# Kernel optimization log

Hardware: AMD Instinct MI355X
Metric: run time of the kernel (lower is better)

The kernel has to match this reference:

```python
import jax, jax.numpy as jnp
import numpy as np

N = 100000   # nodes
E = 1600000  # directed edges
F_IN = 100
H = 256
N_LABELS = 19
BN_EPS = 1e-5


def setup_inputs() -> dict:
    key = jax.random.key(0)
    ks = jax.random.split(key, 12)
    p = lambda k, shape, s=0.05: jax.random.normal(k, shape, dtype=jnp.float32) * s
    return {
        "x": jax.random.normal(ks[0], (N, F_IN), dtype=jnp.float32),
        "edge_index": jax.random.randint(ks[1], (2, E), 0, N, dtype=jnp.int32),
        "W1": p(ks[2], (F_IN, F_IN)), "b1": jnp.zeros((F_IN,), jnp.float32),
        "W2": p(ks[3], (F_IN, F_IN)), "b2": jnp.zeros((F_IN,), jnp.float32),
        "W3": p(ks[4], (F_IN, H)),   "b3": jnp.zeros((H,), jnp.float32),
        "fc1_W": p(ks[5], (H, H)),   "fc1_b": jnp.zeros((H,), jnp.float32),
        "fc2a_W": p(ks[6], (H, 128)), "fc2a_b": jnp.zeros((128,), jnp.float32),
        "bn_gamma": jnp.ones((128,), jnp.float32), "bn_beta": jnp.zeros((128,), jnp.float32),
        "fc2b_W": p(ks[7], (128, N_LABELS)), "fc2b_b": jnp.zeros((N_LABELS,), jnp.float32),
    }


def _gcn_conv(x, W, b, src, dst, dinv):
    """PyG GCNConv with add_self_loops + symmetric normalization.
    out[dst] += dinv[src]*dinv[dst] * (x @ W)[src], plus self-loop term, plus bias.
    """
    n = x.shape[0]
    xw = x @ W  # [N, out]
    norm = dinv[src] * dinv[dst]  # [E]
    agg = jax.ops.segment_sum(xw[src] * norm[:, None], dst, num_segments=n)
    agg = agg + xw * (dinv * dinv)[:, None]  # self loops (i -> i)
    return agg + b


def reference(x, edge_index, W1, b1, W2, b2, W3, b3, fc1_W, fc1_b,
              fc2a_W, fc2a_b, bn_gamma, bn_beta, fc2b_W, fc2b_b):
    src, dst = edge_index[0], edge_index[1]
    n = x.shape[0]
    # degree of augmented graph (A + I), computed on targets (sum aggregation)
    deg = jax.ops.segment_sum(jnp.ones((src.shape[0],), x.dtype), dst, num_segments=n) + 1.0
    dinv = jax.lax.rsqrt(deg)

    h = jnp.clip(x, -0.4, 0.4)
    h = jax.nn.relu(_gcn_conv(h, W1, b1, src, dst, dinv))
    h = jax.nn.relu(_gcn_conv(h, W2, b2, src, dst, dinv))
    h = jax.nn.relu(_gcn_conv(h, W3, b3, src, dst, dinv))
    h = jax.nn.relu(h @ fc1_W + fc1_b)
    # fc2: Linear -> BatchNorm1d (train mode, batch stats) -> ReLU -> Linear
    h = h @ fc2a_W + fc2a_b
    mu = jnp.mean(h, axis=0)
    var = jnp.mean(jnp.square(h - mu), axis=0)  # biased var, as torch BN uses
    h = (h - mu) * jax.lax.rsqrt(var + BN_EPS) * bn_gamma + bn_beta
    h = jax.nn.relu(h)
    logits = h @ fc2b_W + fc2b_b
    return jax.nn.log_softmax(logits, axis=1)
```

## Files before the change

kernel.cpp:

```cpp
#include <hip/hip_runtime.h>
#include <hip/hip_bf16.h>

#define N_NODES 100000
#define N_EDGES 1600000
#define F_IN_DIM 100
#define F_IN_PAD 104
#define H_DIM 256
#define BN_DIM 128
#define N_LABELS 19
#define BN_EPS 1e-5f
#define M_PAD 100096

#define BUCKET_SHIFT 8
#define NB 391
#define EPB 4096
#define PB 391

typedef __attribute__((ext_vector_type(8))) short bf16x8;
typedef __attribute__((ext_vector_type(4))) short s16x4;
typedef __attribute__((ext_vector_type(4))) float f32x4;

static __device__ inline short f2bf(float f) {
    __hip_bfloat16 h = __float2bfloat16(f);
    return *(short*)&h;
}
static __device__ inline float bf2f(short s) {
    unsigned u = ((unsigned)(unsigned short)s) << 16;
    return __builtin_bit_cast(float, u);
}

#define GLOAD_LDS16(g, l) \
    __builtin_amdgcn_global_load_lds((__attribute__((address_space(1))) const unsigned int*)(g), \
                                     (__attribute__((address_space(3))) unsigned int*)(l), 16, 0, 0)

__global__ __launch_bounds__(256) void part_hist_kernel(const int* __restrict__ dst,
                                                        int* __restrict__ part_hist, int E)
{
    __shared__ int h[NB];
    int tid = threadIdx.x;
    for (int i = tid; i < NB; i += 256) h[i] = 0;
    __syncthreads();
    int base = blockIdx.x * EPB;
    int end = min(base + EPB, E);
    for (int e = base + tid; e < end; e += 256)
        atomicAdd(&h[dst[e] >> BUCKET_SHIFT], 1);
    __syncthreads();
    for (int i = tid; i < NB; i += 256) part_hist[blockIdx.x * NB + i] = h[i];
}

__global__ __launch_bounds__(512) void bucket_total_kernel(const int* __restrict__ part_hist,
                                                           int* __restrict__ bucket_total)
{
    __shared__ int ls[512];
    int b = blockIdx.x;
    int s = 0;
    for (int p = threadIdx.x; p < PB; p += 512) s += part_hist[p * NB + b];
    ls[threadIdx.x] = s;
    __syncthreads();
    for (int off = 256; off > 0; off >>= 1) {
        if (threadIdx.x < off) ls[threadIdx.x] += ls[threadIdx.x + off];
        __syncthreads();
    }
    if (threadIdx.x == 0) bucket_total[b] = ls[0];
}

__global__ __launch_bounds__(512) void bucket_scan_kernel(const int* __restrict__ bucket_total,
                                                          int* __restrict__ bucket_base)
{
    __shared__ int ls[512];
    int tid = threadIdx.x;
    ls[tid] = (tid < NB) ? bucket_total[tid] : 0;
    __syncthreads();
    for (int off = 1; off < 512; off <<= 1) {
        int v = ls[tid];
        int add = (tid >= off) ? ls[tid - off] : 0;
        __syncthreads();
        ls[tid] = v + add;
        __syncthreads();
    }
    if (tid < NB) bucket_base[tid] = (tid > 0) ? ls[tid - 1] : 0;
    if (tid == 0) bucket_base[NB] = ls[NB - 1];
}

__global__ __launch_bounds__(512) void part_offset_kernel(int* __restrict__ part_hist,
                                                          const int* __restrict__ bucket_base)
{
    __shared__ int ls[512];
    int b = blockIdx.x;
    int tid = threadIdx.x;
    int v = (tid < PB) ? part_hist[tid * NB + b] : 0;
    ls[tid] = v;
    __syncthreads();
    for (int off = 1; off < 512; off <<= 1) {
        int x = ls[tid];
        int add = (tid >= off) ? ls[tid - off] : 0;
        __syncthreads();
        ls[tid] = x + add;
        __syncthreads();
    }
    if (tid < PB) part_hist[tid * NB + b] = bucket_base[b] + ((tid > 0) ? ls[tid - 1] : 0);
}

__global__ __launch_bounds__(256) void partition_kernel(const int* __restrict__ src,
                                                        const int* __restrict__ dst,
                                                        const int* __restrict__ part_hist,
                                                        int* __restrict__ ep, int E)
{
    __shared__ int cur[NB];
    int tid = threadIdx.x;
    for (int i = tid; i < NB; i += 256) cur[i] = part_hist[blockIdx.x * NB + i];
    __syncthreads();
    int base = blockIdx.x * EPB;
    int end = min(base + EPB, E);
    for (int e = base + tid; e < end; e += 256) {
        int d = dst[e];
        int s = src[e];
        int pos = atomicAdd(&cur[d >> BUCKET_SHIFT], 1);
        ep[pos] = (s << 8) | (d & 255);
    }
}

__global__ __launch_bounds__(256) void bucket_csr_kernel(const int* __restrict__ ep,
                                                         const int* __restrict__ bucket_base,
                                                         int* __restrict__ row_start,
                                                         float* __restrict__ dinv,
                                                         int* __restrict__ src_sorted, int N, int E)
{
    __shared__ int h[256], sc[256], cur[256];
    int b = blockIdx.x;
    int tid = threadIdx.x;
    int e0 = bucket_base[b], e1 = bucket_base[b + 1];
    int node0 = b << BUCKET_SHIFT;
    int nn = min(256, N - node0);

    h[tid] = 0;
    __syncthreads();
    for (int e = e0 + tid; e < e1; e += 256)
        atomicAdd(&h[ep[e] & 255], 1);
    __syncthreads();

    sc[tid] = h[tid];
    __syncthreads();
    for (int off = 1; off < 256; off <<= 1) {
        int v = sc[tid];
        int add = (tid >= off) ? sc[tid - off] : 0;
        __syncthreads();
        sc[tid] = v + add;
        __syncthreads();
    }
    int excl = e0 + ((tid > 0) ? sc[tid - 1] : 0);
    if (tid < nn) {
        row_start[node0 + tid] = excl;
        dinv[node0 + tid] = rsqrtf((float)h[tid] + 1.0f);
    }
    cur[tid] = excl;
    __syncthreads();
    for (int e = e0 + tid; e < e1; e += 256) {
        int p = ep[e];
        int pos = atomicAdd(&cur[p & 255], 1);
        src_sorted[pos] = ((unsigned)p) >> 8;
    }
    if (b == 0 && tid == 0) row_start[N] = E;
}

__global__ __launch_bounds__(256) void pack_all(
    const float* __restrict__ W1, const float* __restrict__ W2, const float* __restrict__ W3,
    const float* __restrict__ Wf1, const float* __restrict__ Wf2a,
    short* __restrict__ Wt1, short* __restrict__ Wt2, short* __restrict__ Wt3,
    short* __restrict__ Wtf1, short* __restrict__ Wtf2a)
{
    int idx = blockIdx.x * 256 + threadIdx.x;
    const float* W; short* Wt; int K, N, Kp, local;
    if (idx < 10400)       { W = W1;   Wt = Wt1;   K = 100; N = 100; Kp = 104; local = idx; }
    else if (idx < 20800)  { W = W2;   Wt = Wt2;   K = 100; N = 100; Kp = 104; local = idx - 10400; }
    else if (idx < 47424)  { W = W3;   Wt = Wt3;   K = 100; N = 256; Kp = 104; local = idx - 20800; }
    else if (idx < 112960) { W = Wf1;  Wt = Wtf1;  K = 256; N = 256; Kp = 256; local = idx - 47424; }
    else if (idx < 145728) { W = Wf2a; Wt = Wtf2a; K = 256; N = 128; Kp = 256; local = idx - 112960; }
    else return;
    int n = local / Kp, k = local - n * Kp;
    Wt[local] = (k < K) ? f2bf(W[(size_t)k * N + n]) : (short)0;
}

template<int ABF16>
__global__ __launch_bounds__(256) void gemm_oneshot(
    const void* __restrict__ Av, const short* __restrict__ Wt,
    const float* __restrict__ bias, const float* __restrict__ rowscale,
    short* __restrict__ C, int M, int Nout, int strideA, int strideC, int relu)
{
    __shared__ __align__(16) short As[128][F_IN_PAD];
    __shared__ __align__(16) short Bs[128][F_IN_PAD];
    int tid = threadIdx.x;
    int rowBase = blockIdx.x * 128;
    int colBase = blockIdx.y * 128;

    if (ABF16) {
        const short* A = (const short*)Av;
        for (int ch = tid; ch < 128 * 13; ch += 256) {
            int r = ch / 13, c8 = (ch - r * 13) * 8;
            int gr = rowBase + r;
            bf16x8 o = (bf16x8){0,0,0,0,0,0,0,0};
            if (gr < M) o = *(const bf16x8*)(A + (size_t)gr * strideA + c8);
            *(bf16x8*)(&As[r][c8]) = o;
        }
    } else {
        const float* A = (const float*)Av;
        for (int ch = tid; ch < 128 * 25; ch += 256) {
            int r = ch / 25, c4 = (ch - r * 25) * 4;
            int gr = rowBase + r;
            float4 v = make_float4(0.f, 0.f, 0.f, 0.f);
            if (gr < M) v = *(const float4*)(A + (size_t)gr * strideA + c4);
            v.x = fminf(fmaxf(v.x, -0.4f), 0.4f);
            v.y = fminf(fmaxf(v.y, -0.4f), 0.4f);
            v.z = fminf(fmaxf(v.z, -0.4f), 0.4f);
            v.w = fminf(fmaxf(v.w, -0.4f), 0.4f);
            s16x4 o = (s16x4){f2bf(v.x), f2bf(v.y), f2bf(v.z), f2bf(v.w)};
            *(s16x4*)(&As[r][c4]) = o;
        }
        for (int r = tid; r < 128; r += 256)
            *(s16x4*)(&As[r][100]) = (s16x4){0, 0, 0, 0};
    }
    for (int ch = tid; ch < 128 * 13; ch += 256) {
        int n = ch / 13, c8 = (ch - n * 13) * 8;
        int gn = colBase + n;
        bf16x8 o = (bf16x8){0,0,0,0,0,0,0,0};
        if (gn < Nout) o = *(const bf16x8*)(Wt + (size_t)gn * F_IN_PAD + c8);
        *(bf16x8*)(&Bs[n][c8]) = o;
    }
    __syncthreads();

    int wid = tid >> 6;
    int lane = tid & 63;
    int quad = lane >> 4, l15 = lane & 15;
    int wave_m = (wid & 1) * 64;
    int wave_n = (wid >> 1) * 64;

    f32x4 acc[4][4];
    #pragma unroll
    for (int i = 0; i < 4; i++)
        #pragma unroll
        for (int j = 0; j < 4; j++)
            acc[i][j] = (f32x4){0.f, 0.f, 0.f, 0.f};

    #pragma unroll
    for (int kc = 0; kc < 4; kc++) {
        int off = kc * 32 + quad * 8;
        bool ok = (off + 8 <= F_IN_PAD);
        bf16x8 a[4], b[4];
        #pragma unroll
        for (int im = 0; im < 4; im++)
            a[im] = ok ? *(const bf16x8*)(&As[wave_m + im * 16 + l15][off])
                       : (bf16x8){0,0,0,0,0,0,0,0};
        #pragma unroll
        for (int in = 0; in < 4; in++)
            b[in] = ok ? *(const bf16x8*)(&Bs[wave_n + in * 16 + l15][off])
                       : (bf16x8){0,0,0,0,0,0,0,0};
        #pragma unroll
        for (int im = 0; im < 4; im++)
            #pragma unroll
            for (int in = 0; in < 4; in++)
                acc[im][in] = __builtin_amdgcn_mfma_f32_16x16x32_bf16(
                    a[im], b[in], acc[im][in], 0, 0, 0);
    }

    #pragma unroll
    for (int im = 0; im < 4; im++) {
        #pragma unroll
        for (int reg = 0; reg < 4; reg++) {
            int row = rowBase + wave_m + im * 16 + quad * 4 + reg;
            if (row >= M) continue;
            float rs = rowscale ? rowscale[row] : 1.f;
            #pragma unroll
            for (int in = 0; in < 4; in++) {
                int col = colBase + wave_n + in * 16 + l15;
                if (col >= strideC) continue;
                float v = 0.f;
                if (col < Nout) {
                    v = acc[im][in][reg];
                    if (bias) v += bias[col];
                    v *= rs;
                    if (relu) v = fmaxf(v, 0.f);
                }
                C[(size_t)row * strideC + col] = f2bf(v);
            }
        }
    }
}

__global__ __launch_bounds__(512, 4) void fc_fused_kernel(
    const short* __restrict__ A,
    const short* __restrict__ W1t,
    const float* __restrict__ b1v,
    const short* __restrict__ W2t,
    const float* __restrict__ b2v,
    short* __restrict__ C)
{
    __shared__ __align__(16) short SB[128 * 256];
    int tid = threadIdx.x;
    int wid = tid >> 6;
    int lane = tid & 63;
    int quad = lane >> 4, l15 = lane & 15;
    int rowBase = blockIdx.x * 128;
    int xr = (l15 & 7) << 4;

    #pragma unroll
    for (int i = 0; i < 8; i++) {
        int c = i * 8 + wid;
        int r = c * 2 + (lane >> 5);
        int pb = ((lane & 31) * 16) ^ ((r & 7) << 4);
        const short* gp = A + (size_t)(rowBase + r) * H_DIM + (pb >> 1);
        GLOAD_LDS16(gp, SB + c * 512);
    }

    int wm = (wid & 1) * 64;
    int wn = (wid >> 1) * 64;

    f32x4 acc[4][4];
    #pragma unroll
    for (int i = 0; i < 4; i++)
        #pragma unroll
        for (int j = 0; j < 4; j++)
            acc[i][j] = (f32x4){0.f, 0.f, 0.f, 0.f};

    bf16x8 bA[4], bB[4];
    auto g1loadB = [&](bf16x8 (&dst)[4], int ks) {
        #pragma unroll
        for (int in = 0; in < 4; in++)
            dst[in] = *(const bf16x8*)(W1t + (size_t)(wn + in * 16 + l15) * H_DIM
                                       + ks * 32 + quad * 8);
    };
    auto g1step = [&](bf16x8 (&bc)[4], int ks) {
        bf16x8 a_[4];
        #pragma unroll
        for (int im = 0; im < 4; im++)
            a_[im] = *(const bf16x8*)(SB + (wm + im * 16 + l15) * 256
                                      + (((ks * 64 + quad * 16) ^ xr) >> 1));
        #pragma unroll
        for (int im = 0; im < 4; im++)
            #pragma unroll
            for (int in = 0; in < 4; in++)
                acc[im][in] = __builtin_amdgcn_mfma_f32_16x16x32_bf16(
                    bc[in], a_[im], acc[im][in], 0, 0, 0);
    };

    g1loadB(bA, 0);
    __syncthreads();

    g1loadB(bB, 1); g1step(bA, 0);
    g1loadB(bA, 2); g1step(bB, 1);
    g1loadB(bB, 3); g1step(bA, 2);
    g1loadB(bA, 4); g1step(bB, 3);
    g1loadB(bB, 5); g1step(bA, 4);
    g1loadB(bA, 6); g1step(bB, 5);
    g1loadB(bB, 7); g1step(bA, 6);
    g1step(bB, 7);

    float bb1[4][4];
    #pragma unroll
    for (int in = 0; in < 4; in++)
        #pragma unroll
        for (int r = 0; r < 4; r++)
            bb1[in][r] = b1v[wn + in * 16 + quad * 4 + r];

    __syncthreads();

    int wm2 = (wid & 1) * 64;
    int wn2 = (wid >> 1) * 32;
    bf16x8 cA[2], cB[2];
    auto g2loadB = [&](bf16x8 (&dst)[2], int ks) {
        #pragma unroll
        for (int in = 0; in < 2; in++)
            dst[in] = *(const bf16x8*)(W2t + (size_t)(wn2 + in * 16 + l15) * H_DIM
                                       + ks * 32 + quad * 8);
    };
    g2loadB(cA, 0);
    float bb2[2] = { b2v[wn2 + l15], b2v[wn2 + 16 + l15] };

    #pragma unroll
    for (int im = 0; im < 4; im++) {
        int ml = wm + im * 16 + l15;
        #pragma unroll
        for (int in = 0; in < 4; in++) {
            int nb = (wn + in * 16 + quad * 4) * 2;
            s16x4 o = (s16x4){
                f2bf(fmaxf(acc[im][in][0] + bb1[in][0], 0.f)),
                f2bf(fmaxf(acc[im][in][1] + bb1[in][1], 0.f)),
                f2bf(fmaxf(acc[im][in][2] + bb1[in][2], 0.f)),
                f2bf(fmaxf(acc[im][in][3] + bb1[in][3], 0.f))};
            *(s16x4*)(SB + ml * 256 + ((nb ^ xr) >> 1)) = o;
        }
    }
    __syncthreads();

    f32x4 acc2[4][2];
    #pragma unroll
    for (int i = 0; i < 4; i++)
        #pragma unroll
        for (int j = 0; j < 2; j++)
            acc2[i][j] = (f32x4){0.f, 0.f, 0.f, 0.f};

    auto g2step = [&](bf16x8 (&bc)[2], int ks) {
        bf16x8 a_[4];
        #pragma unroll
        for (int im = 0; im < 4; im++)
            a_[im] = *(const bf16x8*)(SB + (wm2 + im * 16 + l15) * 256
                                      + (((ks * 64 + quad * 16) ^ xr) >> 1));
        #pragma unroll
        for (int im = 0; im < 4; im++)
            #pragma unroll
            for (int in = 0; in < 2; in++)
                acc2[im][in] = __builtin_amdgcn_mfma_f32_16x16x32_bf16(
                    a_[im], bc[in], acc2[im][in], 0, 0, 0);
    };

    g2loadB(cB, 1); g2step(cA, 0);
    g2loadB(cA, 2); g2step(cB, 1);
    g2loadB(cB, 3); g2step(cA, 2);
    g2loadB(cA, 4); g2step(cB, 3);
    g2loadB(cB, 5); g2step(cA, 4);
    g2loadB(cA, 6); g2step(cB, 5);
    g2loadB(cB, 7); g2step(cA, 6);
    g2step(cB, 7);

    #pragma unroll
    for (int im = 0; im < 4; im++) {
        #pragma unroll
        for (int reg = 0; reg < 4; reg++) {
            int row = rowBase + wm2 + im * 16 + quad * 4 + reg;
            #pragma unroll
            for (int in = 0; in < 2; in++) {
                int col = wn2 + in * 16 + l15;
                C[(size_t)row * BN_DIM + col] = f2bf(acc2[im][in][reg] + bb2[in]);
            }
        }
    }
}

template<int F, int STRIDE, int T, int MODE>
__global__ void gather_kernel(const short* __restrict__ xws,
                              const int* __restrict__ row_start,
                              const int* __restrict__ src_sorted,
                              const float* __restrict__ dinv,
                              const float* __restrict__ bias,
                              short* __restrict__ out, int n)
{
    constexpr int CHUNKS = STRIDE / 8;
    int group = (blockIdx.x * blockDim.x + threadIdx.x) / T;
    int lane = threadIdx.x % T;
    if (group >= n || lane >= CHUNKS) return;
    int d = group;
    int e0 = row_start[d], e1 = row_start[d + 1];
    int coff = lane * 8;
    const short* base = xws + coff;

    float acc[8] = {}, acc2[8] = {};
    int e = e0;
    for (; e + 3 < e1; e += 4) {
        int s0 = src_sorted[e + 0];
        int s1 = src_sorted[e + 1];
        int s2 = src_sorted[e + 2];
        int s3 = src_sorted[e + 3];
        bf16x8 v0 = *(const bf16x8*)(base + (size_t)s0 * STRIDE);
        bf16x8 v1 = *(const bf16x8*)(base + (size_t)s1 * STRIDE);
        bf16x8 v2 = *(const bf16x8*)(base + (size_t)s2 * STRIDE);
        bf16x8 v3 = *(const bf16x8*)(base + (size_t)s3 * STRIDE);
        #pragma unroll
        for (int j = 0; j < 8; j++) {
            acc[j]  += bf2f(v0[j]) + bf2f(v2[j]);
            acc2[j] += bf2f(v1[j]) + bf2f(v3[j]);
        }
    }
    for (; e < e1; e++) {
        int s = src_sorted[e];
        bf16x8 v = *(const bf16x8*)(base + (size_t)s * STRIDE);
        #pragma unroll
        for (int j = 0; j < 8; j++) acc[j] += bf2f(v[j]);
    }

    bf16x8 xv = *(const bf16x8*)(xws + (size_t)d * STRIDE + coff);
    float di = dinv[d];
    bf16x8 o;
    #pragma unroll
    for (int j = 0; j < 8; j++) {
        int col = coff + j;
        float v = 0.f;
        if (col < F) {
            v = di * (acc[j] + acc2[j] + bf2f(xv[j]));
            if (MODE == 0) v = fmaxf(v + bias[col], 0.f);
            if (MODE == 1) v = di * fmaxf(v + bias[col], 0.f);
        }
        o[j] = f2bf(v);
    }
    *(bf16x8*)(out + (size_t)d * STRIDE + coff) = o;
}

__global__ void bn_stats_kernel(const short* __restrict__ h,
                                float* __restrict__ sum, float* __restrict__ sumsq, int Ntot)
{
    int c = threadIdx.x & 127;
    int rpb = blockDim.x >> 7;
    int r0 = blockIdx.x * rpb + (threadIdx.x >> 7);
    int stride = gridDim.x * rpb;
    float s = 0.f, ss = 0.f;
    for (int r = r0; r < Ntot; r += stride) {
        float v = bf2f(h[(size_t)r * BN_DIM + c]);
        s += v; ss += v * v;
    }
    __shared__ float ls[256], lss[256];
    ls[threadIdx.x] = s; lss[threadIdx.x] = ss;
    __syncthreads();
    if (threadIdx.x < 128) {
        s = ls[threadIdx.x] + ls[threadIdx.x + 128];
        ss = lss[threadIdx.x] + lss[threadIdx.x + 128];
        atomicAdd(&sum[c], s);
        atomicAdd(&sumsq[c], ss);
    }
}

__global__ void bn_finalize_kernel(const float* __restrict__ sum, const float* __restrict__ sumsq,
                                   const float* __restrict__ gamma, const float* __restrict__ beta,
                                   float* __restrict__ a, float* __restrict__ b, int Ntot)
{
    int c = threadIdx.x;
    float inv_n = 1.0f / (float)Ntot;
    float mu = sum[c] * inv_n;
    float var = sumsq[c] * inv_n - mu * mu;
    float ai = gamma[c] * rsqrtf(var + BN_EPS);
    a[c] = ai;
    b[c] = beta[c] - mu * ai;
}

__global__ __launch_bounds__(256) void fc2b_fused_kernel(
    const short* __restrict__ h, const float* __restrict__ bn_a, const float* __restrict__ bn_b,
    const float* __restrict__ W, const float* __restrict__ bias,
    float* __restrict__ out, int Ntot)
{
    __shared__ float Ws[BN_DIM][N_LABELS + 1];
    __shared__ float as[BN_DIM], bs[BN_DIM];
    for (int i = threadIdx.x; i < BN_DIM * N_LABELS; i += 256) {
        int k = i / N_LABELS, j = i - k * N_LABELS;
        Ws[k][j] = W[i];
    }
    if (threadIdx.x < BN_DIM) {
        as[threadIdx.x] = bn_a[threadIdx.x];
        bs[threadIdx.x] = bn_b[threadIdx.x];
    }
    __syncthreads();

    int r = blockIdx.x * 256 + threadIdx.x;
    if (r >= Ntot) return;

    float acc[N_LABELS];
    #pragma unroll
    for (int j = 0; j < N_LABELS; j++) acc[j] = bias[j];

    const short* hr = h + (size_t)r * BN_DIM;
    #pragma unroll
    for (int k0 = 0; k0 < BN_DIM; k0 += 8) {
        bf16x8 hv = *(const bf16x8*)(hr + k0);
        #pragma unroll
        for (int t = 0; t < 8; t++) {
            float v = fmaxf(bf2f(hv[t]) * as[k0 + t] + bs[k0 + t], 0.f);
            #pragma unroll
            for (int j = 0; j < N_LABELS; j++)
                acc[j] = fmaf(v, Ws[k0 + t][j], acc[j]);
        }
    }

    float m = acc[0];
    #pragma unroll
    for (int j = 1; j < N_LABELS; j++) m = fmaxf(m, acc[j]);
    float s = 0.f;
    #pragma unroll
    for (int j = 0; j < N_LABELS; j++) s += expf(acc[j] - m);
    float lse = m + logf(s);
    float* o = out + (size_t)r * N_LABELS;
    #pragma unroll
    for (int j = 0; j < N_LABELS; j++) o[j] = acc[j] - lse;
}

extern "C" void kernel_launch(void* const* d_in, const int* in_sizes, int n_in,
                              void* d_out, int out_size, void* d_ws, size_t ws_size,
                              hipStream_t stream)
{
    const float* x      = (const float*)d_in[0];
    const int*   ei     = (const int*)d_in[1];
    const float* W1     = (const float*)d_in[2];
    const float* b1     = (const float*)d_in[3];
    const float* W2     = (const float*)d_in[4];
    const float* b2     = (const float*)d_in[5];
    const float* W3     = (const float*)d_in[6];
    const float* b3     = (const float*)d_in[7];
    const float* fc1_W  = (const float*)d_in[8];
    const float* fc1_b  = (const float*)d_in[9];
    const float* fc2aW  = (const float*)d_in[10];
    const float* fc2ab  = (const float*)d_in[11];
    const float* gamma  = (const float*)d_in[12];
    const float* beta   = (const float*)d_in[13];
    const float* fc2bW  = (const float*)d_in[14];
    const float* fc2bb  = (const float*)d_in[15];
    float* out = (float*)d_out;

    const int* src = ei;
    const int* dst = ei + N_EDGES;

    char* w = (char*)d_ws;
    float* dinv        = (float*)w;  w += ((size_t)N_NODES * 4 + 255) / 256 * 256;
    int*   row_start   = (int*)w;    w += ((size_t)(N_NODES + 1) * 4 + 255) / 256 * 256;
    int*   part_hist   = (int*)w;    w += ((size_t)PB * NB * 4 + 255) / 256 * 256;
    int*   bucket_total= (int*)w;    w += ((size_t)NB * 4 + 255) / 256 * 256;
    int*   bucket_base = (int*)w;    w += ((size_t)(NB + 1) * 4 + 255) / 256 * 256;
    float* bn_sum      = (float*)w;  w += 128 * 4;
    float* bn_sumsq    = (float*)w;  w += 128 * 4;
    float* bn_a        = (float*)w;  w += 128 * 4;
    float* bn_b        = (float*)w;  w += 128 * 4;
    short* Wt1         = (short*)w;  w += ((size_t)F_IN_DIM * F_IN_PAD * 2 + 255) / 256 * 256;
    short* Wt2         = (short*)w;  w += ((size_t)F_IN_DIM * F_IN_PAD * 2 + 255) / 256 * 256;
    short* Wt3         = (short*)w;  w += ((size_t)H_DIM * F_IN_PAD * 2 + 255) / 256 * 256;
    short* Wtf1        = (short*)w;  w += ((size_t)H_DIM * H_DIM * 2 + 255) / 256 * 256;
    short* Wtf2a       = (short*)w;  w += ((size_t)BN_DIM * H_DIM * 2 + 255) / 256 * 256;
    int*   src_sorted  = (int*)w;    w += ((size_t)N_EDGES * 4 + 255) / 256 * 256;
    int*   ep          = (int*)w;    w += ((size_t)N_EDGES * 4 + 255) / 256 * 256;
    short* xws100      = (short*)w;  w += ((size_t)N_NODES * F_IN_PAD * 2 + 255) / 256 * 256;
    short* agg100      = (short*)w;  w += ((size_t)N_NODES * F_IN_PAD * 2 + 255) / 256 * 256;
    short* big1        = (short*)w;  w += ((size_t)M_PAD * H_DIM * 2 + 255) / 256 * 256;
    short* big2        = (short*)w;  w += ((size_t)M_PAD * H_DIM * 2 + 255) / 256 * 256;

    part_hist_kernel<<<PB, 256, 0, stream>>>(dst, part_hist, N_EDGES);
    bucket_total_kernel<<<NB, 512, 0, stream>>>(part_hist, bucket_total);
    bucket_scan_kernel<<<1, 512, 0, stream>>>(bucket_total, bucket_base);
    part_offset_kernel<<<NB, 512, 0, stream>>>(part_hist, bucket_base);
    partition_kernel<<<PB, 256, 0, stream>>>(src, dst, part_hist, ep, N_EDGES);
    bucket_csr_kernel<<<NB, 256, 0, stream>>>(ep, bucket_base, row_start, dinv,
                                              src_sorted, N_NODES, N_EDGES);

    pack_all<<<570, 256, 0, stream>>>(W1, W2, W3, fc1_W, fc2aW, Wt1, Wt2, Wt3, Wtf1, Wtf2a);

    const int nOne = (N_NODES + 127) / 128;
    int gatherBlocks = (N_NODES * 16 + 255) / 256;

    gemm_oneshot<0><<<dim3(nOne, 1), 256, 0, stream>>>(
        x, Wt1, nullptr, dinv, xws100, N_NODES, F_IN_DIM, F_IN_DIM, F_IN_PAD, 0);
    gather_kernel<F_IN_DIM, F_IN_PAD, 16, 0><<<gatherBlocks, 256, 0, stream>>>(
        xws100, row_start, src_sorted, dinv, b1, agg100, N_NODES);

    gemm_oneshot<1><<<dim3(nOne, 1), 256, 0, stream>>>(
        agg100, Wt2, nullptr, dinv, xws100, N_NODES, F_IN_DIM, F_IN_PAD, F_IN_PAD, 0);
    gather_kernel<F_IN_DIM, F_IN_PAD, 16, 1><<<gatherBlocks, 256, 0, stream>>>(
        xws100, row_start, src_sorted, dinv, b2, agg100, N_NODES);

    gather_kernel<F_IN_DIM, F_IN_PAD, 16, 2><<<gatherBlocks, 256, 0, stream>>>(
        agg100, row_start, src_sorted, dinv, nullptr, xws100, N_NODES);
    gemm_oneshot<1><<<dim3(nOne, 2), 256, 0, stream>>>(
        xws100, Wt3, b3, nullptr, big1, N_NODES, H_DIM, F_IN_PAD, H_DIM, 1);

    fc_fused_kernel<<<nOne, 512, 0, stream>>>(
        big1, Wtf1, fc1_b, Wtf2a, fc2ab, big2);

    hipMemsetAsync(bn_sum, 0, 2 * 128 * 4, stream);
    bn_stats_kernel<<<512, 256, 0, stream>>>(big2, bn_sum, bn_sumsq, N_NODES);
    bn_finalize_kernel<<<1, 128, 0, stream>>>(bn_sum, bn_sumsq, gamma, beta, bn_a, bn_b, N_NODES);

    fc2b_fused_kernel<<<(N_NODES + 255) / 256, 256, 0, stream>>>(
        big2, bn_a, bn_b, fc2bW, fc2bb, out, N_NODES);
}
```

Measured before the change: 608.0 us.

## Fuse BatchNorm statistics into fc kernel epilogue and unroll gather by eight

BatchNorm column sums and sums of squares are now accumulated in the fc_fused_kernel epilogue. Each block reduces them through shared-memory atomics and then adds them to global memory. This removes the separate bn_stats_kernel pass that re-read the 100k x 128 activation tensor. The gather kernel is also unrolled to eight outstanding row loads per iteration, with a binary tail and 32-bit byte-offset addressing, to raise memory-level parallelism. The cost is extra epilogue work and shared-memory atomics in the fc kernel, plus higher register pressure in the gather.

Result: slower. 643.2 us (+5.8%).

```diff
diff --git a/kernel.cpp b/kernel.cpp
--- a/kernel.cpp
+++ b/kernel.cpp
@@ -292,7 +292,8 @@
     const float* __restrict__ b1v,
     const short* __restrict__ W2t,
     const float* __restrict__ b2v,
-    short* __restrict__ C)
+    short* __restrict__ C,
+    float* __restrict__ bn_sum, float* __restrict__ bn_sumsq)
 {
     __shared__ __align__(16) short SB[128 * 256];
     int tid = threadIdx.x;
@@ -421,17 +422,41 @@
     g2loadB(cB, 7); g2step(cA, 6);
     g2step(cB, 7);
 
+    float st_s[2] = {0.f, 0.f}, st_ss[2] = {0.f, 0.f};
     #pragma unroll
     for (int im = 0; im < 4; im++) {
         #pragma unroll
         for (int reg = 0; reg < 4; reg++) {
             int row = rowBase + wm2 + im * 16 + quad * 4 + reg;
+            bool live = (row < N_NODES);
             #pragma unroll
             for (int in = 0; in < 2; in++) {
                 int col = wn2 + in * 16 + l15;
-                C[(size_t)row * BN_DIM + col] = f2bf(acc2[im][in][reg] + bb2[in]);
+                short ob = f2bf(acc2[im][in][reg] + bb2[in]);
+                C[(size_t)row * BN_DIM + col] = ob;
+                if (live) {
+                    float v = bf2f(ob);
+                    st_s[in] += v;
+                    st_ss[in] += v * v;
+                }
             }
         }
+    }
+
+    float* red = (float*)SB;
+    __syncthreads();
+    if (tid < 256) red[tid] = 0.f;
+    __syncthreads();
+    #pragma unroll
+    for (int in = 0; in < 2; in++) {
+        int col = wn2 + in * 16 + l15;
+        atomicAdd(&red[col], st_s[in]);
+        atomicAdd(&red[col + 128], st_ss[in]);
+    }
+    __syncthreads();
+    if (tid < 128) {
+        atomicAdd(&bn_sum[tid], red[tid]);
+        atomicAdd(&bn_sumsq[tid], red[tid + 128]);
     }
 }
 
@@ -444,40 +469,70 @@
                               short* __restrict__ out, int n)
 {
     constexpr int CHUNKS = STRIDE / 8;
+    constexpr unsigned ROWB = STRIDE * 2;
     int group = (blockIdx.x * blockDim.x + threadIdx.x) / T;
     int lane = threadIdx.x % T;
     if (group >= n || lane >= CHUNKS) return;
     int d = group;
     int e0 = row_start[d], e1 = row_start[d + 1];
-    int coff = lane * 8;
-    const short* base = xws + coff;
+    const char* base = (const char*)xws + lane * 16;
 
     float acc[8] = {}, acc2[8] = {};
     int e = e0;
-    for (; e + 3 < e1; e += 4) {
-        int s0 = src_sorted[e + 0];
-        int s1 = src_sorted[e + 1];
-        int s2 = src_sorted[e + 2];
-        int s3 = src_sorted[e + 3];
-        bf16x8 v0 = *(const bf16x8*)(base + (size_t)s0 * STRIDE);
-        bf16x8 v1 = *(const bf16x8*)(base + (size_t)s1 * STRIDE);
-        bf16x8 v2 = *(const bf16x8*)(base + (size_t)s2 * STRIDE);
-        bf16x8 v3 = *(const bf16x8*)(base + (size_t)s3 * STRIDE);
+    for (; e + 7 < e1; e += 8) {
+        int s0 = src_sorted[e + 0], s1 = src_sorted[e + 1];
+        int s2 = src_sorted[e + 2], s3 = src_sorted[e + 3];
+        int s4 = src_sorted[e + 4], s5 = src_sorted[e + 5];
+        int s6 = src_sorted[e + 6], s7 = src_sorted[e + 7];
+        bf16x8 v0 = *(const bf16x8*)(base + (unsigned)s0 * ROWB);
+        bf16x8 v1 = *(const bf16x8*)(base + (unsigned)s1 * ROWB);
+        bf16x8 v2 = *(const bf16x8*)(base + (unsigned)s2 * ROWB);
+        bf16x8 v3 = *(const bf16x8*)(base + (unsigned)s3 * ROWB);
+        bf16x8 v4 = *(const bf16x8*)(base + (unsigned)s4 * ROWB);
+        bf16x8 v5 = *(const bf16x8*)(base + (unsigned)s5 * ROWB);
+        bf16x8 v6 = *(const bf16x8*)(base + (unsigned)s6 * ROWB);
+        bf16x8 v7 = *(const bf16x8*)(base + (unsigned)s7 * ROWB);
+        #pragma unroll
+        for (int j = 0; j < 8; j++) {
+            acc[j]  += (bf2f(v0[j]) + bf2f(v2[j])) + (bf2f(v4[j]) + bf2f(v6[j]));
+            acc2[j] += (bf2f(v1[j]) + bf2f(v3[j])) + (bf2f(v5[j]) + bf2f(v7[j]));
+        }
+    }
+    if (e + 3 < e1) {
+        int s0 = src_sorted[e + 0], s1 = src_sorted[e + 1];
+        int s2 = src_sorted[e + 2], s3 = src_sorted[e + 3];
+        bf16x8 v0 = *(const bf16x8*)(base + (unsigned)s0 * ROWB);
+        bf16x8 v1 = *(const bf16x8*)(base + (unsigned)s1 * ROWB);
+        bf16x8 v2 = *(const bf16x8*)(base + (unsigned)s2 * ROWB);
+        bf16x8 v3 = *(const bf16x8*)(base + (unsigned)s3 * ROWB);
         #pragma unroll
         for (int j = 0; j < 8; j++) {
             acc[j]  += bf2f(v0[j]) + bf2f(v2[j]);
             acc2[j] += bf2f(v1[j]) + bf2f(v3[j]);
         }
-    }
-    for (; e < e1; e++) {
-        int s = src_sorted[e];
-        bf16x8 v = *(const bf16x8*)(base + (size_t)s * STRIDE);
-        #pragma unroll
-        for (int j = 0; j < 8; j++) acc[j] += bf2f(v[j]);
-    }
-
-    bf16x8 xv = *(const bf16x8*)(xws + (size_t)d * STRIDE + coff);
+        e += 4;
+    }
+    if (e + 1 < e1) {
+        int s0 = src_sorted[e + 0], s1 = src_sorted[e + 1];
+        bf16x8 v0 = *(const bf16x8*)(base + (unsigned)s0 * ROWB);
+        bf16x8 v1 = *(const bf16x8*)(base + (unsigned)s1 * ROWB);
+        #pragma unroll
+        for (int j = 0; j < 8; j++) {
+            acc[j]  += bf2f(v0[j]);
+            acc2[j] += bf2f(v1[j]);
+        }
+        e += 2;
+    }
+    if (e < e1) {
+        int s0 = src_sorted[e];
+        bf16x8 v0 = *(const bf16x8*)(base + (unsigned)s0 * ROWB);
+        #pragma unroll
+        for (int j = 0; j < 8; j++) acc[j] += bf2f(v0[j]);
+    }
+
+    bf16x8 xv = *(const bf16x8*)(base + (unsigned)d * ROWB);
     float di = dinv[d];
+    int coff = lane * 8;
     bf16x8 o;
     #pragma unroll
     for (int j = 0; j < 8; j++) {
@@ -491,29 +546,6 @@
         o[j] = f2bf(v);
     }
     *(bf16x8*)(out + (size_t)d * STRIDE + coff) = o;
-}
-
-__global__ void bn_stats_kernel(const short* __restrict__ h,
-                                float* __restrict__ sum, float* __restrict__ sumsq, int Ntot)
-{
-    int c = threadIdx.x & 127;
-    int rpb = blockDim.x >> 7;
-    int r0 = blockIdx.x * rpb + (threadIdx.x >> 7);
-    int stride = gridDim.x * rpb;
-    float s = 0.f, ss = 0.f;
-    for (int r = r0; r < Ntot; r += stride) {
-        float v = bf2f(h[(size_t)r * BN_DIM + c]);
-        s += v; ss += v * v;
-    }
-    __shared__ float ls[256], lss[256];
-    ls[threadIdx.x] = s; lss[threadIdx.x] = ss;
-    __syncthreads();
-    if (threadIdx.x < 128) {
-        s = ls[threadIdx.x] + ls[threadIdx.x + 128];
-        ss = lss[threadIdx.x] + lss[threadIdx.x + 128];
-        atomicAdd(&sum[c], s);
-        atomicAdd(&sumsq[c], ss);
-    }
 }
 
 __global__ void bn_finalize_kernel(const float* __restrict__ sum, const float* __restrict__ sumsq,
@@ -653,11 +685,10 @@
     gemm_oneshot<1><<<dim3(nOne, 2), 256, 0, stream>>>(
         xws100, Wt3, b3, nullptr, big1, N_NODES, H_DIM, F_IN_PAD, H_DIM, 1);
 
+    hipMemsetAsync(bn_sum, 0, 2 * 128 * 4, stream);
     fc_fused_kernel<<<nOne, 512, 0, stream>>>(
-        big1, Wtf1, fc1_b, Wtf2a, fc2ab, big2);
-
-    hipMemsetAsync(bn_sum, 0, 2 * 128 * 4, stream);
-    bn_stats_kernel<<<512, 256, 0, stream>>>(big2, bn_sum, bn_sumsq, N_NODES);
+        big1, Wtf1, fc1_b, Wtf2a, fc2ab, big2, bn_sum, bn_sumsq);
+
     bn_finalize_kernel<<<1, 128, 0, stream>>>(bn_sum, bn_sumsq, gamma, beta, bn_a, bn_b, N_NODES);
 
     fc2b_fused_kernel<<<(N_NODES + 255) / 256, 256, 0, stream>>>(
```
